# Optimization experiments

Measured on AMD Instinct MI355X. Metric: run time of the kernel, lower is better.

The kernel has to match this reference:

```python
import jax, jax.numpy as jnp
import numpy as np

B, S, HID, H = 8, 128, 256, 4
DH = HID // H
FF = 4 * HID


def setup_inputs() -> dict:
    key = jax.random.key(0)
    ks = jax.random.split(key, 16)
    n = lambda i, shape: jax.random.normal(ks[i], shape, dtype=jnp.float32) * 0.02
    z = lambda shape: jnp.zeros(shape, dtype=jnp.float32)
    return dict(
        x=jax.random.normal(ks[0], (B, S, HID), dtype=jnp.float32),
        attention_mask=jnp.zeros((B, 1, S, S), dtype=jnp.float32),
        Wq=n(1, (HID, HID)), bq=z((HID,)),
        Wk=n(2, (HID, HID)), bk=z((HID,)),
        Wv=n(3, (HID, HID)), bv=z((HID,)),
        order_w=n(4, (2 * DH,)), order_b=z(()),
        dist_w=n(5, (2 * DH,)), dist_b=z(()),
        scalar=jax.random.normal(ks[6], (1,), dtype=jnp.float32),
        AWq=n(7, (HID, HID)), Abq=z((HID,)),
        AWk=n(8, (HID, HID)), Abk=z((HID,)),
        Wd=n(9, (HID, HID)), bd=z((HID,)),
        g1=jnp.ones((HID,), jnp.float32), beta1=z((HID,)),
        W1=n(10, (HID, FF)), b1=z((FF,)),
        W2=n(11, (FF, HID)), b2=z((HID,)),
        g2=jnp.ones((HID,), jnp.float32), beta2=z((HID,)),
    )


def _ln(t, g, b, eps=1e-12):
    m = t.mean(-1, keepdims=True)
    v = ((t - m) ** 2).mean(-1, keepdims=True)
    return (t - m) / jnp.sqrt(v + eps) * g + b


def _heads(t):
    # [B,S,HID] -> [B,H,S,DH]
    return t.reshape(B, S, H, DH).transpose(0, 2, 1, 3)


def reference(x, attention_mask, Wq, bq, Wk, bk, Wv, bv, order_w, order_b,
              dist_w, dist_b, scalar, AWq, Abq, AWk, Abk, Wd, bd,
              g1, beta1, W1, b1, W2, b2, g2, beta2):
    inv = 1.0 / jnp.sqrt(jnp.float32(DH))
    q = x @ Wq + bq
    k = x @ Wk + bk
    v = x @ Wv + bv
    qh, kh, vh = _heads(q), _heads(k), _heads(v)
    scores = jnp.einsum('bhqd,bhkd->bhqk', qh, kh)  # [B,H,S,S]

    # order/distance affines on concat(q_i, k_j): Linear(2*DH,1) decomposes into
    # per-token projections summed via broadcast (same math, no [B,H,S,S,2*DH] tensor)
    pr_order = jax.nn.sigmoid((qh @ order_w[:DH])[..., :, None]
                              + (kh @ order_w[DH:])[..., None, :] + order_b)
    gd_order = jnp.triu(jnp.ones((S, S), jnp.float32), k=1)
    err_order = (jnp.log(pr_order + 1e-24) * gd_order
                 + jnp.log(1.0 - pr_order + 1e-24) * (1.0 - gd_order))

    idx = jnp.arange(S)
    gd_dist = jnp.log(jnp.abs(idx[None, :] - idx[:, None]).astype(jnp.float32) + 1.0)
    pr_dist = ((qh @ dist_w[:DH])[..., :, None]
               + (kh @ dist_w[DH:])[..., None, :] + dist_b)
    err_dist = -jnp.square(gd_dist - pr_dist) * jnp.square(scalar[0]) * 0.5

    rich_scores = scores + err_order + err_dist
    softm = lambda s: jax.nn.softmax(s * inv + attention_mask, axis=-1)
    rich_probs = softm(rich_scores)
    origin_probs = softm(scores)

    # rich/calibrated combine ('fixed'): softmax(origin + 0.5 * rich)
    combined = jax.nn.softmax(origin_probs + 0.5 * rich_probs, axis=-1)

    # two-level attack attention on transformed mixed q/k
    aq, ak = _heads(q @ AWq + Abq), _heads(k @ AWk + Abk)
    attack_probs = softm(jnp.einsum('bhqd,bhkd->bhqk', aq, ak))
    final_probs = jax.nn.softmax(combined + 0.5 * attack_probs, axis=-1)

    ctx = jnp.einsum('bhqk,bhkd->bhqd', final_probs, vh)
    ctx = ctx.transpose(0, 2, 1, 3).reshape(B, S, HID)
    h = _ln(ctx @ Wd + bd + x, g1, beta1)
    f = jax.nn.gelu(h @ W1 + b1, approximate=False) @ W2 + b2
    return _ln(f + h, g2, beta2)
```

## Files before the change

### kernel.cpp

```cpp
#include <hip/hip_runtime.h>
#include <math.h>

#define B_  8
#define S_  128
#define HID_ 256
#define H_  4
#define DH_ 64
#define FF_ 1024
#define M_  (B_ * S_)

typedef _Float16 half_t;
typedef __attribute__((ext_vector_type(8))) _Float16 half8;
typedef __attribute__((ext_vector_type(4))) float floatx4;

enum { EP_F32 = 0, EP_F16 = 1, EP_F16B = 2, EP_GELU = 3, EP_PROJ = 4 };

__device__ __forceinline__ floatx4 mfma16(half8 a, half8 b, floatx4 c) {
    return __builtin_amdgcn_mfma_f32_16x16x32_f16(a, b, c, 0, 0, 0);
}

__device__ __forceinline__ float qred_sum(float v) {
#pragma unroll
    for (int o = 1; o < 16; o <<= 1) v += __shfl_xor(v, o, 64);
    return v;
}
__device__ __forceinline__ float wred64(float v) {
#pragma unroll
    for (int o = 1; o < 64; o <<= 1) v += __shfl_xor(v, o, 64);
    return v;
}
__device__ __forceinline__ void sm8(float (&v)[8]) {
    float s = 0.f;
#pragma unroll
    for (int j = 0; j < 8; ++j) { v[j] = __expf(v[j]); s += v[j]; }
    s = qred_sum(s);
    float r = 1.f / s;
#pragma unroll
    for (int j = 0; j < 8; ++j) v[j] *= r;
}

template<int EPI, int KLEN>
__device__ __forceinline__ void mgemm(
    half8 (&Asf)[2][4][64], half8 (&Bsf)[2][4][64],
    const half_t* __restrict__ A, int ldA,
    const half_t* __restrict__ Bt, int ldB,
    int m0, int n0,
    const float* __restrict__ bias,
    float* __restrict__ Cf, half_t* __restrict__ Ch, int ldC,
    const float* __restrict__ pw1, const float* __restrict__ pw2,
    float* __restrict__ po1, float* __restrict__ po2, int hsel,
    int tidp)
{
    constexpr int kt = KLEN >> 5;
    const int w = tidp >> 6, l = tidp & 63;
    const int sr = tidp >> 2;
    const int sq = tidp & 3;
    const int sdst = (sr & 15) | (sq << 4);
    const int smt = sr >> 4;
    const half_t* Ap = A + (size_t)(m0 + sr) * ldA + sq * 8;
    const half_t* Bp = Bt + (size_t)(n0 + sr) * ldB + sq * 8;

    half8 ra[kt], rb[kt];
#pragma unroll
    for (int t = 0; t < kt; ++t) {
        ra[t] = *(const half8*)(Ap + t * 32);
        rb[t] = *(const half8*)(Bp + t * 32);
    }

    floatx4 zero = {0.f, 0.f, 0.f, 0.f};
    floatx4 acc[4] = {zero, zero, zero, zero};

    Asf[0][smt][sdst] = ra[0];
    Bsf[0][smt][sdst] = rb[0];
    __syncthreads();
#pragma unroll
    for (int t = 0; t < kt; ++t) {
        const int buf = t & 1;
        half8 a = Asf[buf][w][l];
        acc[0] = mfma16(a, Bsf[buf][0][l], acc[0]);
        acc[1] = mfma16(a, Bsf[buf][1][l], acc[1]);
        acc[2] = mfma16(a, Bsf[buf][2][l], acc[2]);
        acc[3] = mfma16(a, Bsf[buf][3][l], acc[3]);
        if (t + 1 < kt) {
            Asf[buf ^ 1][smt][sdst] = ra[t + 1];
            Bsf[buf ^ 1][smt][sdst] = rb[t + 1];
            __syncthreads();
        }
    }

    const int quad = l >> 4, lc = l & 15;
    const int rowb = m0 + w * 16 + quad * 4;
    float bvv[4] = {0.f, 0.f, 0.f, 0.f};
    if (EPI >= EP_F16B) {
#pragma unroll
        for (int nt = 0; nt < 4; ++nt) bvv[nt] = bias[n0 + nt * 16 + lc];
    }
    float pw1v[4], pw2v[4];
    if (EPI == EP_PROJ) {
#pragma unroll
        for (int nt = 0; nt < 4; ++nt) {
            pw1v[nt] = pw1[nt * 16 + lc];
            pw2v[nt] = pw2[nt * 16 + lc];
        }
    }
#pragma unroll
    for (int rr = 0; rr < 4; ++rr) {
        float ov[4];
#pragma unroll
        for (int nt = 0; nt < 4; ++nt) {
            float o = acc[nt][rr];
            if (EPI >= EP_F16B) o += bvv[nt];
            ov[nt] = o;
            const size_t ci = (size_t)(rowb + rr) * ldC + n0 + nt * 16 + lc;
            if (EPI == EP_F32) Cf[ci] = o;
            else Ch[ci] = (half_t)o;
        }
        if (EPI == EP_PROJ) {
            float po = ov[0] * pw1v[0] + ov[1] * pw1v[1] + ov[2] * pw1v[2] + ov[3] * pw1v[3];
            float pd = ov[0] * pw2v[0] + ov[1] * pw2v[1] + ov[2] * pw2v[2] + ov[3] * pw2v[3];
#pragma unroll
            for (int off = 1; off < 16; off <<= 1) {
                po += __shfl_xor(po, off, 64);
                pd += __shfl_xor(pd, off, 64);
            }
            if (lc == 0) {
                const int m = rowb + rr;
                const int idx = ((m >> 7) * H_ + hsel) * S_ + (m & 127);
                po1[idx] = po;
                po2[idx] = pd;
            }
        }
    }
}

__global__ __launch_bounds__(256) void prep_kernel(
    const float* __restrict__ x,
    const float* __restrict__ Wq, const float* __restrict__ Wk,
    const float* __restrict__ Wv, const float* __restrict__ Wd,
    const float* __restrict__ W1, const float* __restrict__ W2,
    const float* __restrict__ AWq, const float* __restrict__ AWk,
    const float* __restrict__ bq, const float* __restrict__ bk,
    const float* __restrict__ Abq, const float* __restrict__ Abk,
    half_t* __restrict__ x16, half_t* __restrict__ WqT, half_t* __restrict__ WkT,
    half_t* __restrict__ WvT, half_t* __restrict__ WdT,
    half_t* __restrict__ W1T, half_t* __restrict__ W2T,
    half_t* __restrict__ WcqT, half_t* __restrict__ WckT,
    float* __restrict__ bcq, float* __restrict__ bck)
{
    __shared__ union {
        half_t tl[64][72];
        struct { half_t As[64][264]; half_t Bs[64][264]; } c;
        float red[4][64];
    } sm;
    const int tid = threadIdx.x;
    const int j = blockIdx.x;

    if (j < 256) {
        const int base = j * 1024 + tid * 4;
        float4 vv = *(const float4*)(x + base);
        x16[base + 0] = (half_t)vv.x;
        x16[base + 1] = (half_t)vv.y;
        x16[base + 2] = (half_t)vv.z;
        x16[base + 3] = (half_t)vv.w;
        return;
    }
    if (j < 448) {
        int t = j - 256;
        const float* src; half_t* dst; int K, N, k0, n0;
        if (t < 64) {
            int m = t >> 4, q = t & 15;
            const float* ins[4] = {Wq, Wk, Wv, Wd};
            half_t* outs[4] = {WqT, WkT, WvT, WdT};
            src = ins[m]; dst = outs[m]; K = 256; N = 256;
            k0 = (q & 3) * 64; n0 = (q >> 2) * 64;
        } else if (t < 128) {
            int q = t - 64; src = W1; dst = W1T; K = 256; N = 1024;
            k0 = (q & 3) * 64; n0 = (q >> 2) * 64;
        } else {
            int q = t - 128; src = W2; dst = W2T; K = 1024; N = 256;
            k0 = (q >> 2) * 64; n0 = (q & 3) * 64;
        }
        const int r = tid >> 2, c0 = (tid & 3) * 16;
#pragma unroll 4
        for (int i = 0; i < 16; ++i)
            sm.tl[c0 + i][r] = (half_t)src[(size_t)(k0 + r) * N + n0 + c0 + i];
        __syncthreads();
#pragma unroll 4
        for (int i = 0; i < 16; ++i)
            dst[(size_t)(n0 + r) * K + k0 + c0 + i] = sm.tl[r][c0 + i];
        return;
    }
    if (j < 480) {
        int t = j - 448;
        const int z = t >> 4, q = t & 15;
        const int m0 = (q >> 2) * 64, n0 = (q & 3) * 64;
        const float* AW = z ? AWk : AWq;
        const float* W  = z ? Wk : Wq;
        half_t* C       = z ? WckT : WcqT;
        {
            const float* srcA = AW + (size_t)tid * HID_ + m0;
#pragma unroll 4
            for (int i = 0; i < 16; ++i) {
                float4 v = *(const float4*)(srcA + i * 4);
                sm.c.As[i * 4 + 0][tid] = (half_t)v.x;
                sm.c.As[i * 4 + 1][tid] = (half_t)v.y;
                sm.c.As[i * 4 + 2][tid] = (half_t)v.z;
                sm.c.As[i * 4 + 3][tid] = (half_t)v.w;
            }
        }
        {
            const int bn = tid >> 2, bc = (tid & 3) * 64;
            const float* srcB = W + (size_t)(n0 + bn) * HID_ + bc;
            half_t* dstB = &sm.c.Bs[bn][bc];
#pragma unroll 4
            for (int i = 0; i < 16; ++i) {
                float4 v = *(const float4*)(srcB + i * 4);
                dstB[i * 4 + 0] = (half_t)v.x;
                dstB[i * 4 + 1] = (half_t)v.y;
                dstB[i * 4 + 2] = (half_t)v.z;
                dstB[i * 4 + 3] = (half_t)v.w;
            }
        }
        __syncthreads();
        const int w = tid >> 6, l = tid & 63;
        const int quad = l >> 4, lc = l & 15;
        const floatx4 zero = {0.f, 0.f, 0.f, 0.f};
        floatx4 acc[4] = {zero, zero, zero, zero};
#pragma unroll
        for (int kt = 0; kt < 8; ++kt) {
            half8 a = *(const half8*)&sm.c.As[w * 16 + lc][kt * 32 + quad * 8];
#pragma unroll
            for (int nt = 0; nt < 4; ++nt) {
                half8 b = *(const half8*)&sm.c.Bs[nt * 16 + lc][kt * 32 + quad * 8];
                acc[nt] = mfma16(a, b, acc[nt]);
            }
        }
#pragma unroll
        for (int nt = 0; nt < 4; ++nt)
#pragma unroll
            for (int rr = 0; rr < 4; ++rr)
                C[(size_t)(m0 + w * 16 + quad * 4 + rr) * HID_ + n0 + nt * 16 + lc] =
                    (half_t)acc[nt][rr];
        return;
    }
    {
        int t = j - 480;
        const int z = t >> 2, xb = t & 3;
        const float* bsrc = z ? bk : bq;
        const float* AW   = z ? AWk : AWq;
        const float* Ab   = z ? Abk : Abq;
        float* bco        = z ? bck : bcq;
        int l = tid & 63, kc = tid >> 6;
        int n = xb * 64 + l;
        float p = 0.f;
#pragma unroll 8
        for (int kk = 0; kk < 64; ++kk) {
            int k = kc * 64 + kk;
            p = fmaf(bsrc[k], AW[(size_t)k * HID_ + n], p);
        }
        sm.red[kc][l] = p;
        __syncthreads();
        if (kc == 0)
            bco[n] = sm.red[0][l] + sm.red[1][l] + sm.red[2][l] + sm.red[3][l] + Ab[n];
    }
}

__global__ __launch_bounds__(256) void xgemm5(
    const half_t* __restrict__ x16,
    const half_t* __restrict__ WqT, const float* __restrict__ bq,
    const half_t* __restrict__ WkT, const float* __restrict__ bk,
    const half_t* __restrict__ WvT, const float* __restrict__ bv,
    const half_t* __restrict__ WcqT, const float* __restrict__ bcq,
    const half_t* __restrict__ WckT, const float* __restrict__ bck,
    const float* __restrict__ order_w, const float* __restrict__ dist_w,
    half_t* __restrict__ q16, half_t* __restrict__ k16, half_t* __restrict__ v16,
    half_t* __restrict__ aq16, half_t* __restrict__ ak16,
    float* __restrict__ qoA, float* __restrict__ qdA,
    float* __restrict__ koA, float* __restrict__ kdA)
{
    __shared__ half8 Asf[2][4][64], Bsf[2][4][64];
    const int j = blockIdx.x;
    const int z = j >> 6, q = j & 63;
    const int m0 = (q >> 2) * 64, n0 = (q & 3) * 64, bx = q & 3;
    if (z == 0)
        mgemm<EP_PROJ, 256>(Asf, Bsf, x16, HID_, WqT, HID_, m0, n0,
                            bq, nullptr, q16, HID_, order_w, dist_w, qoA, qdA, bx,
                            threadIdx.x);
    else if (z == 1)
        mgemm<EP_PROJ, 256>(Asf, Bsf, x16, HID_, WkT, HID_, m0, n0,
                            bk, nullptr, k16, HID_, order_w + DH_, dist_w + DH_,
                            koA, kdA, bx, threadIdx.x);
    else if (z == 2)
        mgemm<EP_F16B, 256>(Asf, Bsf, x16, HID_, WvT, HID_, m0, n0,
                            bv, nullptr, v16, HID_, nullptr, nullptr, nullptr, nullptr, 0,
                            threadIdx.x);
    else if (z == 3)
        mgemm<EP_F16B, 256>(Asf, Bsf, x16, HID_, WcqT, HID_, m0, n0,
                            bcq, nullptr, aq16, HID_, nullptr, nullptr, nullptr, nullptr, 0,
                            threadIdx.x);
    else
        mgemm<EP_F16B, 256>(Asf, Bsf, x16, HID_, WckT, HID_, m0, n0,
                            bck, nullptr, ak16, HID_, nullptr, nullptr, nullptr, nullptr, 0,
                            threadIdx.x);
}

__global__ __launch_bounds__(64) void attn_kernel(
    const half_t* __restrict__ q16, const half_t* __restrict__ k16,
    const half_t* __restrict__ v16, const half_t* __restrict__ aq16,
    const half_t* __restrict__ ak16,
    const float* __restrict__ qoA, const float* __restrict__ qdA,
    const float* __restrict__ koA, const float* __restrict__ kdA,
    const float* __restrict__ mask,
    const float* __restrict__ order_b_p, const float* __restrict__ dist_b_p,
    const float* __restrict__ scalar_p,
    half_t* __restrict__ ctx16)
{
    __shared__ half8 Kf[2][8][64], AKf[2][8][64];
    __shared__ half_t Vt[64][136];
    __shared__ half_t Pm[16][136];

    const int l = threadIdx.x;
    const int quad = l >> 4, lc = l & 15;
    const int bh = blockIdx.x >> 3, rt = blockIdx.x & 7;
    const int b = bh >> 2, h = bh & 3;
    const size_t hoff = (size_t)b * S_ * HID_ + (size_t)h * DH_;

#pragma unroll
    for (int u = 0; u < 16; ++u) {
        int idx = u * 64 + l;
        int j = idx >> 3, c = idx & 7;
        size_t g = hoff + (size_t)j * HID_ + c * 8;
        int kt = c >> 2, jt = j >> 4, sl = (j & 15) | ((c & 3) << 4);
        Kf[kt][jt][sl]  = *(const half8*)(k16 + g);
        AKf[kt][jt][sl] = *(const half8*)(ak16 + g);
    }
#pragma unroll
    for (int u = 0; u < 16; ++u) {
        int j = (u >> 3) * 64 + l;
        int c = u & 7;
        half8 vv = *(const half8*)(v16 + hoff + (size_t)j * HID_ + c * 8);
#pragma unroll
        for (int e = 0; e < 8; ++e) Vt[c * 8 + e][j] = vv[e];
    }
    __syncthreads();

    half8 qf[2], aqf[2];
#pragma unroll
    for (int kt = 0; kt < 2; ++kt) {
        size_t g = hoff + (size_t)(rt * 16 + lc) * HID_ + kt * 32 + quad * 8;
        qf[kt]  = *(const half8*)(q16 + g);
        aqf[kt] = *(const half8*)(aq16 + g);
    }
    floatx4 zero = {0.f, 0.f, 0.f, 0.f};
    floatx4 accS[8], accA[8];
#pragma unroll
    for (int jt = 0; jt < 8; ++jt) { accS[jt] = zero; accA[jt] = zero; }
#pragma unroll
    for (int kt = 0; kt < 2; ++kt) {
#pragma unroll
        for (int jt = 0; jt < 8; ++jt) {
            accS[jt] = mfma16(qf[kt], Kf[kt][jt][l], accS[jt]);
            accA[jt] = mfma16(aqf[kt], AKf[kt][jt][l], accA[jt]);
        }
    }

    const float ob = order_b_p[0], db = dist_b_p[0];
    const float scl = scalar_p[0];
    const float s2 = scl * scl;
    const float inv = 0.125f;
    float kov[8], kdv[8];
#pragma unroll
    for (int jt = 0; jt < 8; ++jt) {
        kov[jt] = koA[bh * S_ + jt * 16 + lc];
        kdv[jt] = kdA[bh * S_ + jt * 16 + lc];
    }
#pragma unroll
    for (int reg = 0; reg < 4; ++reg) {
        const int il = quad * 4 + reg;
        const int i  = rt * 16 + il;
        float qo = qoA[bh * S_ + i], qd = qdA[bh * S_ + i];
        const float* mrow = mask + ((size_t)(b * S_ + i)) * S_;
        float mk[8], lg[8], as_[8];
#pragma unroll
        for (int jt = 0; jt < 8; ++jt) {
            mk[jt] = mrow[jt * 16 + lc];
            lg[jt] = accS[jt][reg];
            as_[jt] = accA[jt][reg];
        }
        float p0[8];
#pragma unroll
        for (int jt = 0; jt < 8; ++jt) p0[jt] = lg[jt] * inv + mk[jt];
        sm8(p0);
        float p1[8];
#pragma unroll
        for (int jt = 0; jt < 8; ++jt) {
            int j = jt * 16 + lc;
            float pr = 1.f / (1.f + __expf(-(qo + kov[jt] + ob)));
            float sel = (j > i) ? pr : 1.f - pr;
            float erro = __logf(sel + 1e-24f);
            float gd = __logf(fabsf((float)(j - i)) + 1.f);
            float dd = gd - (qd + kdv[jt] + db);
            p1[jt] = (lg[jt] + erro - 0.5f * dd * dd * s2) * inv + mk[jt];
        }
        sm8(p1);
#pragma unroll
        for (int jt = 0; jt < 8; ++jt) p0[jt] += 0.5f * p1[jt];
        sm8(p0);
#pragma unroll
        for (int jt = 0; jt < 8; ++jt) p1[jt] = as_[jt] * inv + mk[jt];
        sm8(p1);
#pragma unroll
        for (int jt = 0; jt < 8; ++jt) p0[jt] += 0.5f * p1[jt];
        sm8(p0);
#pragma unroll
        for (int jt = 0; jt < 8; ++jt) Pm[il][jt * 16 + lc] = (half_t)p0[jt];
    }
    __syncthreads();

    half8 pa_[4];
#pragma unroll
    for (int kt = 0; kt < 4; ++kt)
        pa_[kt] = *(const half8*)&Pm[lc][kt * 32 + quad * 8];
    floatx4 apv[4];
#pragma unroll
    for (int nt = 0; nt < 4; ++nt) apv[nt] = zero;
#pragma unroll
    for (int nt = 0; nt < 4; ++nt) {
#pragma unroll
        for (int kt = 0; kt < 4; ++kt) {
            half8 vf = *(const half8*)&Vt[nt * 16 + lc][kt * 32 + quad * 8];
            apv[nt] = mfma16(pa_[kt], vf, apv[nt]);
        }
    }
#pragma unroll
    for (int nt = 0; nt < 4; ++nt) {
#pragma unroll
        for (int reg = 0; reg < 4; ++reg) {
            int i = rt * 16 + quad * 4 + reg;
            ctx16[hoff + (size_t)i * HID_ + nt * 16 + lc] = (half_t)apv[nt][reg];
        }
    }
}

struct TailSmem {
    half8 Af[8][64];
    float hS[8][257];
    half_t h16L[8][264];
    half_t f116L[8][1032];
};

__global__ __launch_bounds__(512) void tail_kernel(
    const half_t* __restrict__ ctx16, const half_t* __restrict__ WdT,
    const float* __restrict__ x, const float* __restrict__ bd,
    const float* __restrict__ g1, const float* __restrict__ beta1,
    const half_t* __restrict__ W1T, const float* __restrict__ b1,
    const half_t* __restrict__ W2T, const float* __restrict__ b2,
    const float* __restrict__ g2, const float* __restrict__ beta2,
    float* __restrict__ out)
{
    __shared__ TailSmem sm;
    const int tid = threadIdx.x;
    const int r0 = blockIdx.x * 8;
    const int w = tid >> 6, l = tid & 63;
    const int quad = l >> 4, lc = l & 15;
    const floatx4 zero = {0.f, 0.f, 0.f, 0.f};

    {
        int row = tid >> 5, c = tid & 31;
        sm.Af[c >> 2][row | ((c & 3) << 4)] =
            *(const half8*)(ctx16 + (size_t)(r0 + (row & 7)) * HID_ + c * 8);
    }
    __syncthreads();

    {
        const int n0 = w * 32;
        half8 bw[8][2];
#pragma unroll
        for (int kt = 0; kt < 8; ++kt)
#pragma unroll
            for (int nt = 0; nt < 2; ++nt)
                bw[kt][nt] = *(const half8*)(WdT + (size_t)(n0 + nt * 16 + lc) * HID_
                                             + kt * 32 + quad * 8);
        floatx4 acc[2] = {zero, zero};
#pragma unroll
        for (int kt = 0; kt < 8; ++kt) {
            half8 a = sm.Af[kt][l];
            acc[0] = mfma16(a, bw[kt][0], acc[0]);
            acc[1] = mfma16(a, bw[kt][1], acc[1]);
        }
        if (quad < 2) {
#pragma unroll
            for (int nt = 0; nt < 2; ++nt)
#pragma unroll
                for (int rr = 0; rr < 4; ++rr) {
                    int row = quad * 4 + rr, col = n0 + nt * 16 + lc;
                    sm.hS[row][col] = acc[nt][rr] + bd[col]
                                    + x[(size_t)(r0 + row) * HID_ + col];
                }
        }
    }
    __syncthreads();

    {
        const int row = tid >> 6, jj = tid & 63;
        float s = 0.f;
#pragma unroll
        for (int i = 0; i < 4; ++i) s += sm.hS[row][i * 64 + jj];
        s = wred64(s);
        float mean = s * (1.f / 256.f);
        float vs = 0.f;
#pragma unroll
        for (int i = 0; i < 4; ++i) { float d = sm.hS[row][i * 64 + jj] - mean; vs += d * d; }
        vs = wred64(vs);
        float rs = rsqrtf(vs * (1.f / 256.f) + 1e-12f);
#pragma unroll
        for (int i = 0; i < 4; ++i) {
            int col = i * 64 + jj;
            float v = (sm.hS[row][col] - mean) * rs * g1[col] + beta1[col];
            sm.hS[row][col] = v;
            sm.h16L[row][col] = (half_t)v;
        }
    }
    __syncthreads();

#pragma unroll
    for (int nb = 0; nb < 2; ++nb) {
        const int n0 = w * 128 + nb * 64;
        floatx4 acc[4] = {zero, zero, zero, zero};
        half8 bw[2][4][4];
#pragma unroll
        for (int kt = 0; kt < 4; ++kt)
#pragma unroll
            for (int nt = 0; nt < 4; ++nt)
                bw[0][kt][nt] = *(const half8*)(W1T + (size_t)(n0 + nt * 16 + lc) * HID_
                                                + kt * 32 + quad * 8);
#pragma unroll
        for (int c = 0; c < 2; ++c) {
            if (c == 0) {
#pragma unroll
                for (int kt = 0; kt < 4; ++kt)
#pragma unroll
                    for (int nt = 0; nt < 4; ++nt)
                        bw[1][kt][nt] = *(const half8*)(W1T
                            + (size_t)(n0 + nt * 16 + lc) * HID_ + (4 + kt) * 32 + quad * 8);
            }
#pragma unroll
            for (int kt = 0; kt < 4; ++kt) {
                half8 a = *(const half8*)&sm.h16L[l & 7][(c * 4 + kt) * 32 + quad * 8];
#pragma unroll
                for (int nt = 0; nt < 4; ++nt)
                    acc[nt] = mfma16(a, bw[c][kt][nt], acc[nt]);
            }
        }
        if (quad < 2) {
#pragma unroll
            for (int nt = 0; nt < 4; ++nt)
#pragma unroll
                for (int rr = 0; rr < 4; ++rr) {
                    int row = quad * 4 + rr, col = n0 + nt * 16 + lc;
                    float o = acc[nt][rr] + b1[col];
                    o = 0.5f * o * (1.f + erff(o * 0.70710678118654752f));
                    sm.f116L[row][col] = (half_t)o;
                }
        }
    }
    __syncthreads();

    {
        const int n0 = w * 32;
        floatx4 acc[2] = {zero, zero};
        half8 bw[2][4][2];
#pragma unroll
        for (int kt = 0; kt < 4; ++kt)
#pragma unroll
            for (int nt = 0; nt < 2; ++nt)
                bw[0][kt][nt] = *(const half8*)(W2T + (size_t)(n0 + nt * 16 + lc) * FF_
                                                + kt * 32 + quad * 8);
#pragma unroll
        for (int c = 0; c < 8; ++c) {
            if (c < 7) {
#pragma unroll
                for (int kt = 0; kt < 4; ++kt)
#pragma unroll
                    for (int nt = 0; nt < 2; ++nt)
                        bw[(c + 1) & 1][kt][nt] = *(const half8*)(W2T
                            + (size_t)(n0 + nt * 16 + lc) * FF_ + ((c + 1) * 4 + kt) * 32 + quad * 8);
            }
#pragma unroll
            for (int kt = 0; kt < 4; ++kt) {
                half8 a = *(const half8*)&sm.f116L[l & 7][(c * 4 + kt) * 32 + quad * 8];
#pragma unroll
                for (int nt = 0; nt < 2; ++nt)
                    acc[nt] = mfma16(a, bw[c & 1][kt][nt], acc[nt]);
            }
        }
        if (quad < 2) {
#pragma unroll
            for (int nt = 0; nt < 2; ++nt)
#pragma unroll
                for (int rr = 0; rr < 4; ++rr) {
                    int row = quad * 4 + rr, col = n0 + nt * 16 + lc;
                    sm.hS[row][col] = acc[nt][rr] + b2[col] + sm.hS[row][col];
                }
        }
    }
    __syncthreads();

    {
        const int row = tid >> 6, jj = tid & 63;
        float s = 0.f;
#pragma unroll
        for (int i = 0; i < 4; ++i) s += sm.hS[row][i * 64 + jj];
        s = wred64(s);
        float mean = s * (1.f / 256.f);
        float vs = 0.f;
#pragma unroll
        for (int i = 0; i < 4; ++i) { float d = sm.hS[row][i * 64 + jj] - mean; vs += d * d; }
        vs = wred64(vs);
        float rs = rsqrtf(vs * (1.f / 256.f) + 1e-12f);
#pragma unroll
        for (int i = 0; i < 4; ++i) {
            int col = i * 64 + jj;
            out[(size_t)(r0 + row) * HID_ + col] =
                (sm.hS[row][col] - mean) * rs * g2[col] + beta2[col];
        }
    }
}

extern "C" void kernel_launch(void* const* d_in, const int* in_sizes, int n_in,
                              void* d_out, int out_size, void* d_ws, size_t ws_size,
                              hipStream_t stream) {
    const float* x        = (const float*)d_in[0];
    const float* mask     = (const float*)d_in[1];
    const float* Wq       = (const float*)d_in[2];
    const float* bq       = (const float*)d_in[3];
    const float* Wk       = (const float*)d_in[4];
    const float* bk       = (const float*)d_in[5];
    const float* Wv       = (const float*)d_in[6];
    const float* bv       = (const float*)d_in[7];
    const float* order_w  = (const float*)d_in[8];
    const float* order_b  = (const float*)d_in[9];
    const float* dist_w   = (const float*)d_in[10];
    const float* dist_b   = (const float*)d_in[11];
    const float* scalar   = (const float*)d_in[12];
    const float* AWq      = (const float*)d_in[13];
    const float* Abq      = (const float*)d_in[14];
    const float* AWk      = (const float*)d_in[15];
    const float* Abk      = (const float*)d_in[16];
    const float* Wd       = (const float*)d_in[17];
    const float* bd       = (const float*)d_in[18];
    const float* g1       = (const float*)d_in[19];
    const float* beta1    = (const float*)d_in[20];
    const float* W1       = (const float*)d_in[21];
    const float* b1       = (const float*)d_in[22];
    const float* W2       = (const float*)d_in[23];
    const float* b2       = (const float*)d_in[24];
    const float* g2       = (const float*)d_in[25];
    const float* beta2    = (const float*)d_in[26];

    float* ws = (float*)d_ws;
    size_t off = 0;
    auto ahf = [&](size_t nh) { half_t* p = (half_t*)(ws + off); off += nh / 2; return p; };
    auto afl = [&](size_t n) { float* p = ws + off; off += n; return p; };

    half_t* x16   = ahf(M_ * HID_);
    half_t* WqT   = ahf(HID_ * HID_);
    half_t* WkT   = ahf(HID_ * HID_);
    half_t* WvT   = ahf(HID_ * HID_);
    half_t* WdT   = ahf(HID_ * HID_);
    half_t* W1T   = ahf(HID_ * FF_);
    half_t* W2T   = ahf(HID_ * FF_);
    half_t* WcqT  = ahf(HID_ * HID_);
    half_t* WckT  = ahf(HID_ * HID_);
    half_t* q16   = ahf(M_ * HID_);
    half_t* k16   = ahf(M_ * HID_);
    half_t* v16   = ahf(M_ * HID_);
    half_t* aq16  = ahf(M_ * HID_);
    half_t* ak16  = ahf(M_ * HID_);
    half_t* ctx16 = ahf(M_ * HID_);
    float* bcq  = afl(256);
    float* bck  = afl(256);
    float* qoA  = afl(B_ * H_ * S_);
    float* qdA  = afl(B_ * H_ * S_);
    float* koA  = afl(B_ * H_ * S_);
    float* kdA  = afl(B_ * H_ * S_);

    prep_kernel<<<488, 256, 0, stream>>>(
        x, Wq, Wk, Wv, Wd, W1, W2, AWq, AWk, bq, bk, Abq, Abk,
        x16, WqT, WkT, WvT, WdT, W1T, W2T, WcqT, WckT, bcq, bck);
    xgemm5<<<320, 256, 0, stream>>>(
        x16, WqT, bq, WkT, bk, WvT, bv, WcqT, bcq, WckT, bck, order_w, dist_w,
        q16, k16, v16, aq16, ak16, qoA, qdA, koA, kdA);
    attn_kernel<<<256, 64, 0, stream>>>(
        q16, k16, v16, aq16, ak16, qoA, qdA, koA, kdA,
        mask, order_b, dist_b, scalar, ctx16);
    tail_kernel<<<128, 512, 0, stream>>>(
        ctx16, WdT, x, bd, g1, beta1, W1T, b1, W2T, b2, g2, beta2, (float*)d_out);
}
```

Before: 171.0 us.

## Split fused tail into dense+LN1, FF1, split-K FF2, and LN2 kernels

Replaces the single 128-block tail kernel, which processed 8 rows per block and wasted half of each MFMA tile, with four kernels. The new dense+LN1 kernel handles 16 rows per block. The FFN matmuls now reuse the tiled mgemm (GELU added as an epilogue) across 256 and 128 blocks, with FF2 split along K into two partial outputs summed in a separate LN2 kernel. This raises parallelism and MFMA utilisation, at the cost of extra launches and global round-trips for the intermediates.

```diff
diff --git a/kernel.cpp b/kernel.cpp
--- a/kernel.cpp
+++ b/kernel.cpp
@@ -110,6 +110,7 @@
         for (int nt = 0; nt < 4; ++nt) {
             float o = acc[nt][rr];
             if (EPI >= EP_F16B) o += bvv[nt];
+            if (EPI == EP_GELU) o = 0.5f * o * (1.f + erff(o * 0.70710678118654752f));
             ov[nt] = o;
             const size_t ci = (size_t)(rowb + rr) * ldC + n0 + nt * 16 + lc;
             if (EPI == EP_F32) Cf[ci] = o;
@@ -442,33 +443,24 @@
     }
 }
 
-struct TailSmem {
-    half8 Af[8][64];
-    float hS[8][257];
-    half_t h16L[8][264];
-    half_t f116L[8][1032];
-};
-
-__global__ __launch_bounds__(512) void tail_kernel(
+__global__ __launch_bounds__(512) void dense_ln1_kernel(
     const half_t* __restrict__ ctx16, const half_t* __restrict__ WdT,
     const float* __restrict__ x, const float* __restrict__ bd,
     const float* __restrict__ g1, const float* __restrict__ beta1,
-    const half_t* __restrict__ W1T, const float* __restrict__ b1,
-    const half_t* __restrict__ W2T, const float* __restrict__ b2,
-    const float* __restrict__ g2, const float* __restrict__ beta2,
-    float* __restrict__ out)
-{
-    __shared__ TailSmem sm;
+    float* __restrict__ hb32, half_t* __restrict__ h16)
+{
+    __shared__ half8 Af[8][64];
+    __shared__ float hS[16][257];
     const int tid = threadIdx.x;
-    const int r0 = blockIdx.x * 8;
+    const int r0 = blockIdx.x * 16;
     const int w = tid >> 6, l = tid & 63;
     const int quad = l >> 4, lc = l & 15;
     const floatx4 zero = {0.f, 0.f, 0.f, 0.f};
 
     {
         int row = tid >> 5, c = tid & 31;
-        sm.Af[c >> 2][row | ((c & 3) << 4)] =
-            *(const half8*)(ctx16 + (size_t)(r0 + (row & 7)) * HID_ + c * 8);
+        Af[c >> 2][row | ((c & 3) << 4)] =
+            *(const half8*)(ctx16 + (size_t)(r0 + row) * HID_ + c * 8);
     }
     __syncthreads();
 
@@ -484,146 +476,101 @@
         floatx4 acc[2] = {zero, zero};
 #pragma unroll
         for (int kt = 0; kt < 8; ++kt) {
-            half8 a = sm.Af[kt][l];
+            half8 a = Af[kt][l];
             acc[0] = mfma16(a, bw[kt][0], acc[0]);
             acc[1] = mfma16(a, bw[kt][1], acc[1]);
         }
-        if (quad < 2) {
-#pragma unroll
-            for (int nt = 0; nt < 2; ++nt)
-#pragma unroll
-                for (int rr = 0; rr < 4; ++rr) {
-                    int row = quad * 4 + rr, col = n0 + nt * 16 + lc;
-                    sm.hS[row][col] = acc[nt][rr] + bd[col]
-                                    + x[(size_t)(r0 + row) * HID_ + col];
-                }
-        }
+#pragma unroll
+        for (int nt = 0; nt < 2; ++nt)
+#pragma unroll
+            for (int rr = 0; rr < 4; ++rr) {
+                int row = quad * 4 + rr, col = n0 + nt * 16 + lc;
+                hS[row][col] = acc[nt][rr] + bd[col]
+                             + x[(size_t)(r0 + row) * HID_ + col];
+            }
     }
     __syncthreads();
 
     {
-        const int row = tid >> 6, jj = tid & 63;
+        const int row = tid >> 5, jj = tid & 31;
         float s = 0.f;
 #pragma unroll
-        for (int i = 0; i < 4; ++i) s += sm.hS[row][i * 64 + jj];
-        s = wred64(s);
+        for (int i = 0; i < 8; ++i) s += hS[row][i * 32 + jj];
+#pragma unroll
+        for (int o = 1; o < 32; o <<= 1) s += __shfl_xor(s, o, 64);
         float mean = s * (1.f / 256.f);
         float vs = 0.f;
 #pragma unroll
-        for (int i = 0; i < 4; ++i) { float d = sm.hS[row][i * 64 + jj] - mean; vs += d * d; }
-        vs = wred64(vs);
+        for (int i = 0; i < 8; ++i) { float d = hS[row][i * 32 + jj] - mean; vs += d * d; }
+#pragma unroll
+        for (int o = 1; o < 32; o <<= 1) vs += __shfl_xor(vs, o, 64);
         float rs = rsqrtf(vs * (1.f / 256.f) + 1e-12f);
 #pragma unroll
-        for (int i = 0; i < 4; ++i) {
-            int col = i * 64 + jj;
-            float v = (sm.hS[row][col] - mean) * rs * g1[col] + beta1[col];
-            sm.hS[row][col] = v;
-            sm.h16L[row][col] = (half_t)v;
-        }
-    }
-    __syncthreads();
-
-#pragma unroll
-    for (int nb = 0; nb < 2; ++nb) {
-        const int n0 = w * 128 + nb * 64;
-        floatx4 acc[4] = {zero, zero, zero, zero};
-        half8 bw[2][4][4];
-#pragma unroll
-        for (int kt = 0; kt < 4; ++kt)
-#pragma unroll
-            for (int nt = 0; nt < 4; ++nt)
-                bw[0][kt][nt] = *(const half8*)(W1T + (size_t)(n0 + nt * 16 + lc) * HID_
-                                                + kt * 32 + quad * 8);
-#pragma unroll
-        for (int c = 0; c < 2; ++c) {
-            if (c == 0) {
-#pragma unroll
-                for (int kt = 0; kt < 4; ++kt)
-#pragma unroll
-                    for (int nt = 0; nt < 4; ++nt)
-                        bw[1][kt][nt] = *(const half8*)(W1T
-                            + (size_t)(n0 + nt * 16 + lc) * HID_ + (4 + kt) * 32 + quad * 8);
-            }
-#pragma unroll
-            for (int kt = 0; kt < 4; ++kt) {
-                half8 a = *(const half8*)&sm.h16L[l & 7][(c * 4 + kt) * 32 + quad * 8];
-#pragma unroll
-                for (int nt = 0; nt < 4; ++nt)
-                    acc[nt] = mfma16(a, bw[c][kt][nt], acc[nt]);
-            }
-        }
-        if (quad < 2) {
-#pragma unroll
-            for (int nt = 0; nt < 4; ++nt)
-#pragma unroll
-                for (int rr = 0; rr < 4; ++rr) {
-                    int row = quad * 4 + rr, col = n0 + nt * 16 + lc;
-                    float o = acc[nt][rr] + b1[col];
-                    o = 0.5f * o * (1.f + erff(o * 0.70710678118654752f));
-                    sm.f116L[row][col] = (half_t)o;
-                }
-        }
-    }
-    __syncthreads();
-
-    {
-        const int n0 = w * 32;
-        floatx4 acc[2] = {zero, zero};
-        half8 bw[2][4][2];
-#pragma unroll
-        for (int kt = 0; kt < 4; ++kt)
-#pragma unroll
-            for (int nt = 0; nt < 2; ++nt)
-                bw[0][kt][nt] = *(const half8*)(W2T + (size_t)(n0 + nt * 16 + lc) * FF_
-                                                + kt * 32 + quad * 8);
-#pragma unroll
-        for (int c = 0; c < 8; ++c) {
-            if (c < 7) {
-#pragma unroll
-                for (int kt = 0; kt < 4; ++kt)
-#pragma unroll
-                    for (int nt = 0; nt < 2; ++nt)
-                        bw[(c + 1) & 1][kt][nt] = *(const half8*)(W2T
-                            + (size_t)(n0 + nt * 16 + lc) * FF_ + ((c + 1) * 4 + kt) * 32 + quad * 8);
-            }
-#pragma unroll
-            for (int kt = 0; kt < 4; ++kt) {
-                half8 a = *(const half8*)&sm.f116L[l & 7][(c * 4 + kt) * 32 + quad * 8];
-#pragma unroll
-                for (int nt = 0; nt < 2; ++nt)
-                    acc[nt] = mfma16(a, bw[c & 1][kt][nt], acc[nt]);
-            }
-        }
-        if (quad < 2) {
-#pragma unroll
-            for (int nt = 0; nt < 2; ++nt)
-#pragma unroll
-                for (int rr = 0; rr < 4; ++rr) {
-                    int row = quad * 4 + rr, col = n0 + nt * 16 + lc;
-                    sm.hS[row][col] = acc[nt][rr] + b2[col] + sm.hS[row][col];
-                }
-        }
-    }
-    __syncthreads();
-
-    {
-        const int row = tid >> 6, jj = tid & 63;
-        float s = 0.f;
-#pragma unroll
-        for (int i = 0; i < 4; ++i) s += sm.hS[row][i * 64 + jj];
-        s = wred64(s);
-        float mean = s * (1.f / 256.f);
-        float vs = 0.f;
-#pragma unroll
-        for (int i = 0; i < 4; ++i) { float d = sm.hS[row][i * 64 + jj] - mean; vs += d * d; }
-        vs = wred64(vs);
-        float rs = rsqrtf(vs * (1.f / 256.f) + 1e-12f);
-#pragma unroll
-        for (int i = 0; i < 4; ++i) {
-            int col = i * 64 + jj;
-            out[(size_t)(r0 + row) * HID_ + col] =
-                (sm.hS[row][col] - mean) * rs * g2[col] + beta2[col];
-        }
+        for (int i = 0; i < 8; ++i) {
+            int col = i * 32 + jj;
+            float v = (hS[row][col] - mean) * rs * g1[col] + beta1[col];
+            size_t gi = (size_t)(r0 + row) * HID_ + col;
+            hb32[gi] = v;
+            h16[gi] = (half_t)v;
+        }
+    }
+}
+
+__global__ __launch_bounds__(256) void ff1_kernel(
+    const half_t* __restrict__ h16, const half_t* __restrict__ W1T,
+    const float* __restrict__ b1, half_t* __restrict__ f116)
+{
+    __shared__ half8 Asf[2][4][64], Bsf[2][4][64];
+    const int j = blockIdx.x;
+    mgemm<EP_GELU, 256>(Asf, Bsf, h16, HID_, W1T, HID_,
+                        (j >> 4) * 64, (j & 15) * 64,
+                        b1, nullptr, f116, FF_, nullptr, nullptr, nullptr, nullptr, 0,
+                        threadIdx.x);
+}
+
+__global__ __launch_bounds__(256) void ff2_kernel(
+    const half_t* __restrict__ f116, const half_t* __restrict__ W2T,
+    float* __restrict__ pf0, float* __restrict__ pf1)
+{
+    __shared__ half8 Asf[2][4][64], Bsf[2][4][64];
+    const int j = blockIdx.x;
+    const int m0 = (j >> 3) * 64, n0 = ((j >> 1) & 3) * 64, ks = j & 1;
+    float* C = ks ? pf1 : pf0;
+    mgemm<EP_F32, 512>(Asf, Bsf, f116 + ks * 512, FF_, W2T + ks * 512, FF_,
+                       m0, n0,
+                       nullptr, C, nullptr, HID_, nullptr, nullptr, nullptr, nullptr, 0,
+                       threadIdx.x);
+}
+
+__global__ __launch_bounds__(256) void ln2_kernel(
+    const float* __restrict__ pf0, const float* __restrict__ pf1,
+    const float* __restrict__ b2, const float* __restrict__ hb32,
+    const float* __restrict__ g2, const float* __restrict__ beta2,
+    float* __restrict__ out)
+{
+    const int tid = threadIdx.x;
+    const int row = blockIdx.x * 4 + (tid >> 6);
+    const int jj = tid & 63;
+    const size_t base = (size_t)row * HID_;
+    float v[4];
+    float s = 0.f;
+#pragma unroll
+    for (int i = 0; i < 4; ++i) {
+        int col = i * 64 + jj;
+        v[i] = pf0[base + col] + pf1[base + col] + b2[col] + hb32[base + col];
+        s += v[i];
+    }
+    s = wred64(s);
+    float mean = s * (1.f / 256.f);
+    float vs = 0.f;
+#pragma unroll
+    for (int i = 0; i < 4; ++i) { float d = v[i] - mean; vs += d * d; }
+    vs = wred64(vs);
+    float rs = rsqrtf(vs * (1.f / 256.f) + 1e-12f);
+#pragma unroll
+    for (int i = 0; i < 4; ++i) {
+        int col = i * 64 + jj;
+        out[base + col] = (v[i] - mean) * rs * g2[col] + beta2[col];
     }
 }
 
@@ -678,6 +625,11 @@
     half_t* aq16  = ahf(M_ * HID_);
     half_t* ak16  = ahf(M_ * HID_);
     half_t* ctx16 = ahf(M_ * HID_);
+    half_t* h16   = ahf(M_ * HID_);
+    half_t* f116  = ahf(M_ * FF_);
+    float* hb32 = afl(M_ * HID_);
+    float* pf0  = afl(M_ * HID_);
+    float* pf1  = afl(M_ * HID_);
     float* bcq  = afl(256);
     float* bck  = afl(256);
     float* qoA  = afl(B_ * H_ * S_);
@@ -694,6 +646,9 @@
     attn_kernel<<<256, 64, 0, stream>>>(
         q16, k16, v16, aq16, ak16, qoA, qdA, koA, kdA,
         mask, order_b, dist_b, scalar, ctx16);
-    tail_kernel<<<128, 512, 0, stream>>>(
-        ctx16, WdT, x, bd, g1, beta1, W1T, b1, W2T, b2, g2, beta2, (float*)d_out);
-}
+    dense_ln1_kernel<<<64, 512, 0, stream>>>(
+        ctx16, WdT, x, bd, g1, beta1, hb32, h16);
+    ff1_kernel<<<256, 256, 0, stream>>>(h16, W1T, b1, f116);
+    ff2_kernel<<<128, 256, 0, stream>>>(f116, W2T, pf0, pf1);
+    ln2_kernel<<<256, 256, 0, stream>>>(pf0, pf1, b2, hb32, g2, beta2, (float*)d_out);
+}
```

After: 153.3 us. 1.12x faster.
